# Kernel optimization log

Measured on AMD Instinct MI355X. Metric: run time of the kernel, lower is better.

## Reference

```python
import jax, jax.numpy as jnp
import numpy as np

VOCAB, D, PATCH, ROUNDS = 256, 64, 4, 3
B, T = 32, 8192


def setup_inputs() -> dict:
    key = jax.random.key(0)
    ks = jax.random.split(key, 16)
    s = 0.02
    inp = {
        "x": jax.random.randint(ks[0], (B, T), 0, VOCAB),
        "emb": jax.random.normal(ks[1], (VOCAB, D), jnp.float32) * s,
        # msg_net: Linear(2d->d), GELU, Linear(d->d); weights stored [in, out]
        "w_m1": jax.random.normal(ks[2], (2 * D, D), jnp.float32) * s,
        "b_m1": jnp.zeros((D,), jnp.float32),
        "w_m2": jax.random.normal(ks[3], (D, D), jnp.float32) * s,
        "b_m2": jnp.zeros((D,), jnp.float32),
        # update_net: Linear(2d->d), GELU, Linear(d->d)
        "w_u1": jax.random.normal(ks[4], (2 * D, D), jnp.float32) * s,
        "b_u1": jnp.zeros((D,), jnp.float32),
        "w_u2": jax.random.normal(ks[5], (D, D), jnp.float32) * s,
        "b_u2": jnp.zeros((D,), jnp.float32),
        # LayerNorm(d)
        "ln_g": jnp.ones((D,), jnp.float32),
        "ln_b": jnp.zeros((D,), jnp.float32),
        # readout: Linear(d -> vocab)
        "w_r": jax.random.normal(ks[6], (D, VOCAB), jnp.float32) * s,
        "b_r": jnp.zeros((VOCAB,), jnp.float32),
    }
    return inp


def _mlp(z, w1, b1, w2, b2):
    h = jax.nn.gelu(z @ w1 + b1, approximate=False)  # torch nn.GELU default = exact erf
    return h @ w2 + b2


def _layernorm(h, g, b, eps=1e-5):
    mu = jnp.mean(h, axis=-1, keepdims=True)
    var = jnp.mean((h - mu) ** 2, axis=-1, keepdims=True)
    return (h - mu) / jnp.sqrt(var + eps) * g + b


def reference(x, emb, w_m1, b_m1, w_m2, b_m2, w_u1, b_u1, w_u2, b_u2, ln_g, ln_b, w_r, b_r):
    Bx, Tx = x.shape
    P = PATCH
    N = (Tx + P - 1) // P
    xp = jnp.pad(x, ((0, 0), (0, N * P - Tx)))  # pad token id 0
    h = emb[xp].reshape(Bx, N, P, D).mean(axis=2)  # [B, N, d] patch-node features
    for _ in range(ROUNDS):
        left = jnp.pad(h[:, :-1], ((0, 0), (1, 0), (0, 0)))  # shift-right along N
        msgs = _mlp(jnp.concatenate([h, left], axis=-1), w_m1, b_m1, w_m2, b_m2)
        upd = _mlp(jnp.concatenate([h, msgs], axis=-1), w_u1, b_u1, w_u2, b_u2)
        h = _layernorm(h + upd, ln_g, ln_b)
    tok = jnp.repeat(h, P, axis=1)[:, :Tx]  # broadcast node feat to its P tokens
    return tok @ w_r + b_r  # [B, T, vocab]
```

## Files before the change

### kernel.cpp

```cpp
#include <hip/hip_runtime.h>
#include <hip/hip_bf16.h>
#include <math.h>

#define DD 64
#define NPB 2048
#define RTOT 65536
#define W1S 136
#define W2S 72

typedef __bf16 bf16;
typedef bf16 bf16x8 __attribute__((ext_vector_type(8)));
typedef float f32x4 __attribute__((ext_vector_type(4)));

#define COMPILER_FENCE() asm volatile("" ::: "memory")

__device__ __forceinline__ f32x4 mfma16(bf16x8 a, bf16x8 b, f32x4 c) {
  return __builtin_amdgcn_mfma_f32_16x16x32_bf16(a, b, c, 0, 0, 0);
}

__device__ __forceinline__ float gelu_exact(float x) {
  return 0.5f * x * (1.0f + erff(x * 0.70710678118654752f));
}

__device__ __forceinline__ bf16x8 cvt8(const float* p) {
  f32x4 a = *reinterpret_cast<const f32x4*>(p);
  f32x4 b = *reinterpret_cast<const f32x4*>(p + 4);
  bf16x8 r;
  r[0] = (bf16)a[0]; r[1] = (bf16)a[1]; r[2] = (bf16)a[2]; r[3] = (bf16)a[3];
  r[4] = (bf16)b[0]; r[5] = (bf16)b[1]; r[6] = (bf16)b[2]; r[7] = (bf16)b[3];
  return r;
}

__device__ __forceinline__ bf16x8 zero8() {
  bf16x8 z = {(bf16)0.f, (bf16)0.f, (bf16)0.f, (bf16)0.f,
              (bf16)0.f, (bf16)0.f, (bf16)0.f, (bf16)0.f};
  return z;
}

__global__ void __launch_bounds__(256) k_embed(const int* __restrict__ x,
                                               const float* __restrict__ emb,
                                               float* __restrict__ h) {
  int gid = blockIdx.x * 256 + threadIdx.x;
  int row = gid >> 6, d = gid & 63;
  const int* xp = x + row * 4;
  float s = 0.f;
#pragma unroll
  for (int p = 0; p < 4; ++p) s += emb[xp[p] * DD + d];
  h[row * DD + d] = s * 0.25f;
}

__global__ void __launch_bounds__(256) k_prep(const float* __restrict__ wm1,
                                              const float* __restrict__ wm2,
                                              const float* __restrict__ wu1,
                                              const float* __restrict__ wu2,
                                              bf16* __restrict__ Wsc) {
  int gid = blockIdx.x * 256 + threadIdx.x;
  if (gid < 8192) {
    int n = gid >> 7, k = gid & 127;
    Wsc[gid] = (bf16)wm1[k * 64 + n];
  } else if (gid < 16384) {
    int j = gid - 8192, n = j >> 7, k = j & 127;
    Wsc[gid] = (bf16)wu1[k * 64 + n];
  } else if (gid < 20480) {
    int j = gid - 16384, n = j >> 6, k = j & 63;
    Wsc[gid] = (bf16)wm2[k * 64 + n];
  } else {
    int j = gid - 20480, n = j >> 6, k = j & 63;
    Wsc[gid] = (bf16)wu2[k * 64 + n];
  }
}

__global__ void __launch_bounds__(256) k_prep_r(const float* __restrict__ wr,
                                                bf16* __restrict__ wrt) {
  int gid = blockIdx.x * 256 + threadIdx.x;
  int v = gid >> 6, k = gid & 63;
  wrt[gid] = (bf16)wr[k * 256 + v];
}

__global__ void __launch_bounds__(256) k_round_m(const float* __restrict__ hin,
                                                 float* __restrict__ hout,
                                                 const bf16* __restrict__ Wsc,
                                                 const float* __restrict__ bm1,
                                                 const float* __restrict__ bm2,
                                                 const float* __restrict__ bu1,
                                                 const float* __restrict__ bu2,
                                                 const float* __restrict__ lng,
                                                 const float* __restrict__ lnb) {
  __shared__ bf16 W1[2][64 * W1S];
  __shared__ bf16 Ms[64 * W2S];
  __shared__ bf16 Hs[64 * W2S];

  const int tid = threadIdx.x;
  const int lane = tid & 63;
  const int wv = tid >> 6;
  const int l15 = lane & 15;
  const int lhi = lane >> 4;
  const int rowbase = blockIdx.x * 64;

  for (int i = tid; i < 2048; i += 256) {
    int buf = i >> 10, idx = i & 1023;
    int n = idx >> 4, g = (idx & 15) * 8;
    *reinterpret_cast<bf16x8*>(&W1[buf][n * W1S + g]) =
        *reinterpret_cast<const bf16x8*>(Wsc + buf * 8192 + n * 128 + g);
  }
  bf16x8 fm2[4][2], fu2[4][2];
#pragma unroll
  for (int ct = 0; ct < 4; ++ct)
#pragma unroll
    for (int kt = 0; kt < 2; ++kt) {
      int off = (ct * 16 + l15) * 64 + kt * 32 + lhi * 8;
      fm2[ct][kt] = *reinterpret_cast<const bf16x8*>(Wsc + 16384 + off);
      fu2[ct][kt] = *reinterpret_cast<const bf16x8*>(Wsc + 20480 + off);
    }
  float bm1v[4], bm2v[4], bu1v[4], bu2v[4], lngv[4], lnbv[4];
#pragma unroll
  for (int ct = 0; ct < 4; ++ct) {
    int c = ct * 16 + l15;
    bm1v[ct] = bm1[c]; bm2v[ct] = bm2[c];
    bu1v[ct] = bu1[c]; bu2v[ct] = bu2[c];
    lngv[ct] = lng[c]; lnbv[ct] = lnb[c];
  }
  __syncthreads();

  const int lrow = wv * 16 + l15;
  const int grow = rowbase + lrow;
  const float* hrow = hin + (size_t)grow * DD;

  bf16x8 ah0 = cvt8(hrow + lhi * 8);
  bf16x8 ah1 = cvt8(hrow + 32 + lhi * 8);
  bf16x8 al0 = zero8(), al1 = zero8();
  if ((grow & (NPB - 1)) != 0) {
    al0 = cvt8(hrow - DD + lhi * 8);
    al1 = cvt8(hrow - DD + 32 + lhi * 8);
  }

  f32x4 acc[4];
  const f32x4 fz = {0.f, 0.f, 0.f, 0.f};

#pragma unroll
  for (int ct = 0; ct < 4; ++ct) acc[ct] = fz;
#pragma unroll
  for (int ct = 0; ct < 4; ++ct) {
    const bf16* wb = &W1[0][(ct * 16 + l15) * W1S];
    acc[ct] = mfma16(ah0, *reinterpret_cast<const bf16x8*>(wb + lhi * 8), acc[ct]);
    acc[ct] = mfma16(ah1, *reinterpret_cast<const bf16x8*>(wb + 32 + lhi * 8), acc[ct]);
    acc[ct] = mfma16(al0, *reinterpret_cast<const bf16x8*>(wb + 64 + lhi * 8), acc[ct]);
    acc[ct] = mfma16(al1, *reinterpret_cast<const bf16x8*>(wb + 96 + lhi * 8), acc[ct]);
  }
#pragma unroll
  for (int ct = 0; ct < 4; ++ct)
#pragma unroll
    for (int r = 0; r < 4; ++r) {
      float g = gelu_exact(acc[ct][r] + bm1v[ct]);
      Hs[(wv * 16 + lhi * 4 + r) * W2S + ct * 16 + l15] = (bf16)g;
    }
  COMPILER_FENCE();

#pragma unroll
  for (int ct = 0; ct < 4; ++ct) acc[ct] = fz;
  {
    bf16x8 g0 = *reinterpret_cast<const bf16x8*>(&Hs[lrow * W2S + lhi * 8]);
    bf16x8 g1 = *reinterpret_cast<const bf16x8*>(&Hs[lrow * W2S + 32 + lhi * 8]);
#pragma unroll
    for (int ct = 0; ct < 4; ++ct) {
      acc[ct] = mfma16(g0, fm2[ct][0], acc[ct]);
      acc[ct] = mfma16(g1, fm2[ct][1], acc[ct]);
    }
  }
#pragma unroll
  for (int ct = 0; ct < 4; ++ct)
#pragma unroll
    for (int r = 0; r < 4; ++r)
      Ms[(wv * 16 + lhi * 4 + r) * W2S + ct * 16 + l15] =
          (bf16)(acc[ct][r] + bm2v[ct]);
  COMPILER_FENCE();

#pragma unroll
  for (int ct = 0; ct < 4; ++ct) acc[ct] = fz;
  {
    bf16x8 m0 = *reinterpret_cast<const bf16x8*>(&Ms[lrow * W2S + lhi * 8]);
    bf16x8 m1 = *reinterpret_cast<const bf16x8*>(&Ms[lrow * W2S + 32 + lhi * 8]);
#pragma unroll
    for (int ct = 0; ct < 4; ++ct) {
      const bf16* wb = &W1[1][(ct * 16 + l15) * W1S];
      acc[ct] = mfma16(ah0, *reinterpret_cast<const bf16x8*>(wb + lhi * 8), acc[ct]);
      acc[ct] = mfma16(ah1, *reinterpret_cast<const bf16x8*>(wb + 32 + lhi * 8), acc[ct]);
      acc[ct] = mfma16(m0, *reinterpret_cast<const bf16x8*>(wb + 64 + lhi * 8), acc[ct]);
      acc[ct] = mfma16(m1, *reinterpret_cast<const bf16x8*>(wb + 96 + lhi * 8), acc[ct]);
    }
  }
  COMPILER_FENCE();
#pragma unroll
  for (int ct = 0; ct < 4; ++ct)
#pragma unroll
    for (int r = 0; r < 4; ++r) {
      float g = gelu_exact(acc[ct][r] + bu1v[ct]);
      Hs[(wv * 16 + lhi * 4 + r) * W2S + ct * 16 + l15] = (bf16)g;
    }
  COMPILER_FENCE();

#pragma unroll
  for (int ct = 0; ct < 4; ++ct) acc[ct] = fz;
  {
    bf16x8 u0 = *reinterpret_cast<const bf16x8*>(&Hs[lrow * W2S + lhi * 8]);
    bf16x8 u1 = *reinterpret_cast<const bf16x8*>(&Hs[lrow * W2S + 32 + lhi * 8]);
#pragma unroll
    for (int ct = 0; ct < 4; ++ct) {
      acc[ct] = mfma16(u0, fu2[ct][0], acc[ct]);
      acc[ct] = mfma16(u1, fu2[ct][1], acc[ct]);
    }
  }

  float xv[4][4];
#pragma unroll
  for (int ct = 0; ct < 4; ++ct)
#pragma unroll
    for (int r = 0; r < 4; ++r) {
      int row = rowbase + wv * 16 + lhi * 4 + r;
      xv[ct][r] = acc[ct][r] + bu2v[ct] + hin[row * DD + ct * 16 + l15];
    }
  float s1[4], s2[4];
#pragma unroll
  for (int r = 0; r < 4; ++r) {
    s1[r] = 0.f; s2[r] = 0.f;
#pragma unroll
    for (int ct = 0; ct < 4; ++ct) {
      s1[r] += xv[ct][r];
      s2[r] += xv[ct][r] * xv[ct][r];
    }
  }
#pragma unroll
  for (int off = 1; off < 16; off <<= 1)
#pragma unroll
    for (int r = 0; r < 4; ++r) {
      s1[r] += __shfl_xor(s1[r], off);
      s2[r] += __shfl_xor(s2[r], off);
    }
#pragma unroll
  for (int r = 0; r < 4; ++r) {
    float mu = s1[r] * 0.015625f;
    float var = s2[r] * 0.015625f - mu * mu;
    float rstd = rsqrtf(var + 1e-5f);
    int row = rowbase + wv * 16 + lhi * 4 + r;
#pragma unroll
    for (int ct = 0; ct < 4; ++ct)
      hout[row * DD + ct * 16 + l15] =
          (xv[ct][r] - mu) * rstd * lngv[ct] + lnbv[ct];
  }
}

__global__ void __launch_bounds__(256) k_readout(const float* __restrict__ h,
                                                 const bf16* __restrict__ wrt,
                                                 const float* __restrict__ br,
                                                 float* __restrict__ out) {
  __shared__ bf16 Wt[256 * W2S];
  const int tid = threadIdx.x, lane = tid & 63, wv = tid >> 6;
  const int l15 = lane & 15, lhi = lane >> 4;

  for (int i = tid; i < 2048; i += 256) {
    int v = i >> 3, g = (i & 7) * 8;
    *reinterpret_cast<bf16x8*>(&Wt[v * W2S + g]) =
        *reinterpret_cast<const bf16x8*>(wrt + v * 64 + g);
  }
  f32x4 brv[16];
#pragma unroll
  for (int vt = 0; vt < 16; ++vt)
    brv[vt] = *reinterpret_cast<const f32x4*>(br + vt * 16 + lhi * 4);
  __syncthreads();

  const int node = blockIdx.x * 64 + wv * 16 + l15;
  const float* hrow = h + (size_t)node * DD;
  bf16x8 b0 = cvt8(hrow + lhi * 8);
  bf16x8 b1 = cvt8(hrow + 32 + lhi * 8);

  f32x4 acc[16];
  const f32x4 fz = {0.f, 0.f, 0.f, 0.f};
#pragma unroll
  for (int vt = 0; vt < 16; ++vt) {
    const bf16* wb = &Wt[(vt * 16 + l15) * W2S];
    bf16x8 a0 = *reinterpret_cast<const bf16x8*>(wb + lhi * 8);
    bf16x8 a1 = *reinterpret_cast<const bf16x8*>(wb + 32 + lhi * 8);
    acc[vt] = mfma16(a0, b0, fz);
    acc[vt] = mfma16(a1, b1, acc[vt]);
  }

  float* ob = out + (size_t)node * 1024 + lhi * 4;
#pragma unroll
  for (int vt = 0; vt < 16; ++vt) {
    f32x4 val = acc[vt] + brv[vt];
    float* p = ob + vt * 16;
#pragma unroll
    for (int rep = 0; rep < 4; ++rep)
      *reinterpret_cast<f32x4*>(p + rep * 256) = val;
  }
}

extern "C" void kernel_launch(void* const* d_in, const int* in_sizes, int n_in,
                              void* d_out, int out_size, void* d_ws, size_t ws_size,
                              hipStream_t stream) {
  const int*   x   = (const int*)d_in[0];
  const float* emb = (const float*)d_in[1];
  const float* wm1 = (const float*)d_in[2];
  const float* bm1 = (const float*)d_in[3];
  const float* wm2 = (const float*)d_in[4];
  const float* bm2 = (const float*)d_in[5];
  const float* wu1 = (const float*)d_in[6];
  const float* bu1 = (const float*)d_in[7];
  const float* wu2 = (const float*)d_in[8];
  const float* bu2 = (const float*)d_in[9];
  const float* lng = (const float*)d_in[10];
  const float* lnb = (const float*)d_in[11];
  const float* wr  = (const float*)d_in[12];
  const float* br  = (const float*)d_in[13];
  float* out = (float*)d_out;

  char* ws = (char*)d_ws;
  float* ha = (float*)ws;
  float* hb = (float*)(ws + (size_t)RTOT * DD * 4);
  bf16* Wsc = (bf16*)d_out;
  bf16* wrt = (bf16*)ha;

  hipLaunchKernelGGL(k_prep, dim3(96), dim3(256), 0, stream,
                     wm1, wm2, wu1, wu2, Wsc);
  hipLaunchKernelGGL(k_embed, dim3(16384), dim3(256), 0, stream, x, emb, ha);
  hipLaunchKernelGGL(k_round_m, dim3(1024), dim3(256), 0, stream,
                     ha, hb, Wsc, bm1, bm2, bu1, bu2, lng, lnb);
  hipLaunchKernelGGL(k_round_m, dim3(1024), dim3(256), 0, stream,
                     hb, ha, Wsc, bm1, bm2, bu1, bu2, lng, lnb);
  hipLaunchKernelGGL(k_round_m, dim3(1024), dim3(256), 0, stream,
                     ha, hb, Wsc, bm1, bm2, bu1, bu2, lng, lnb);
  hipLaunchKernelGGL(k_prep_r, dim3(64), dim3(256), 0, stream, wr, wrt);
  hipLaunchKernelGGL(k_readout, dim3(1024), dim3(256), 0, stream, hb, wrt, br, out);
}
```

Before: 139.1 us.

## Fuse embed, three message-passing rounds and readout into one halo-tiled kernel

Replaces the separate embed, three round and readout kernels with a single kernel. Each block holds 80 node rows (64 outputs plus a 16-row left halo) in shared memory as bf16 across all rounds, so the per-round fp32 node features never go out to global memory and come back. In exchange, each block recomputes the halo rows, reloads the first-layer weights into shared memory twice per round behind extra barriers, and runs the readout on only 4 of 5 waves in two halves. Weight preparation, including the readout weights, is merged into one prep kernel that writes to workspace.

Result: slower. 156.1 us (+12.2%).

```diff
diff --git a/kernel.cpp b/kernel.cpp
--- a/kernel.cpp
+++ b/kernel.cpp
@@ -7,6 +7,8 @@
 #define RTOT 65536
 #define W1S 136
 #define W2S 72
+#define HBS 136
+#define TROWS 80
 
 typedef __bf16 bf16;
 typedef bf16 bf16x8 __attribute__((ext_vector_type(8)));
@@ -22,13 +24,8 @@
   return 0.5f * x * (1.0f + erff(x * 0.70710678118654752f));
 }
 
-__device__ __forceinline__ bf16x8 cvt8(const float* p) {
-  f32x4 a = *reinterpret_cast<const f32x4*>(p);
-  f32x4 b = *reinterpret_cast<const f32x4*>(p + 4);
-  bf16x8 r;
-  r[0] = (bf16)a[0]; r[1] = (bf16)a[1]; r[2] = (bf16)a[2]; r[3] = (bf16)a[3];
-  r[4] = (bf16)b[0]; r[5] = (bf16)b[1]; r[6] = (bf16)b[2]; r[7] = (bf16)b[3];
-  return r;
+__device__ __forceinline__ bf16x8 ld8(const bf16* p) {
+  return *reinterpret_cast<const bf16x8*>(p);
 }
 
 __device__ __forceinline__ bf16x8 zero8() {
@@ -37,22 +34,11 @@
   return z;
 }
 
-__global__ void __launch_bounds__(256) k_embed(const int* __restrict__ x,
-                                               const float* __restrict__ emb,
-                                               float* __restrict__ h) {
-  int gid = blockIdx.x * 256 + threadIdx.x;
-  int row = gid >> 6, d = gid & 63;
-  const int* xp = x + row * 4;
-  float s = 0.f;
-#pragma unroll
-  for (int p = 0; p < 4; ++p) s += emb[xp[p] * DD + d];
-  h[row * DD + d] = s * 0.25f;
-}
-
 __global__ void __launch_bounds__(256) k_prep(const float* __restrict__ wm1,
                                               const float* __restrict__ wm2,
                                               const float* __restrict__ wu1,
                                               const float* __restrict__ wu2,
+                                              const float* __restrict__ wr,
                                               bf16* __restrict__ Wsc) {
   int gid = blockIdx.x * 256 + threadIdx.x;
   if (gid < 8192) {
@@ -64,54 +50,47 @@
   } else if (gid < 20480) {
     int j = gid - 16384, n = j >> 6, k = j & 63;
     Wsc[gid] = (bf16)wm2[k * 64 + n];
-  } else {
+  } else if (gid < 24576) {
     int j = gid - 20480, n = j >> 6, k = j & 63;
     Wsc[gid] = (bf16)wu2[k * 64 + n];
-  }
-}
-
-__global__ void __launch_bounds__(256) k_prep_r(const float* __restrict__ wr,
-                                                bf16* __restrict__ wrt) {
-  int gid = blockIdx.x * 256 + threadIdx.x;
-  int v = gid >> 6, k = gid & 63;
-  wrt[gid] = (bf16)wr[k * 256 + v];
-}
-
-__global__ void __launch_bounds__(256) k_round_m(const float* __restrict__ hin,
-                                                 float* __restrict__ hout,
-                                                 const bf16* __restrict__ Wsc,
-                                                 const float* __restrict__ bm1,
-                                                 const float* __restrict__ bm2,
-                                                 const float* __restrict__ bu1,
-                                                 const float* __restrict__ bu2,
-                                                 const float* __restrict__ lng,
-                                                 const float* __restrict__ lnb) {
-  __shared__ bf16 W1[2][64 * W1S];
-  __shared__ bf16 Ms[64 * W2S];
-  __shared__ bf16 Hs[64 * W2S];
+  } else {
+    int j = gid - 24576, v = j >> 6, k = j & 63;
+    Wsc[gid] = (bf16)wr[k * 256 + v];
+  }
+}
+
+__global__ void __launch_bounds__(320) k_fused(const int* __restrict__ x,
+                                               const float* __restrict__ emb,
+                                               const bf16* __restrict__ Wsc,
+                                               const float* __restrict__ bm1,
+                                               const float* __restrict__ bm2,
+                                               const float* __restrict__ bu1,
+                                               const float* __restrict__ bu2,
+                                               const float* __restrict__ lng,
+                                               const float* __restrict__ lnb,
+                                               const float* __restrict__ br,
+                                               float* __restrict__ out) {
+  __shared__ __align__(16) char arena[50688];
+  bf16* Hs = (bf16*)arena;
+  bf16* W1 = (bf16*)(arena + 11520);
+  bf16* Hb = (bf16*)(arena + 28928);
+  bf16* Wt = (bf16*)arena;
+
+  const bf16* wm1t = Wsc;
+  const bf16* wu1t = Wsc + 8192;
+  const bf16* wm2t = Wsc + 16384;
+  const bf16* wu2t = Wsc + 20480;
+  const bf16* wrt  = Wsc + 24576;
 
   const int tid = threadIdx.x;
   const int lane = tid & 63;
   const int wv = tid >> 6;
   const int l15 = lane & 15;
   const int lhi = lane >> 4;
-  const int rowbase = blockIdx.x * 64;
-
-  for (int i = tid; i < 2048; i += 256) {
-    int buf = i >> 10, idx = i & 1023;
-    int n = idx >> 4, g = (idx & 15) * 8;
-    *reinterpret_cast<bf16x8*>(&W1[buf][n * W1S + g]) =
-        *reinterpret_cast<const bf16x8*>(Wsc + buf * 8192 + n * 128 + g);
-  }
-  bf16x8 fm2[4][2], fu2[4][2];
-#pragma unroll
-  for (int ct = 0; ct < 4; ++ct)
-#pragma unroll
-    for (int kt = 0; kt < 2; ++kt) {
-      int off = (ct * 16 + l15) * 64 + kt * 32 + lhi * 8;
-      fm2[ct][kt] = *reinterpret_cast<const bf16x8*>(Wsc + 16384 + off);
-      fu2[ct][kt] = *reinterpret_cast<const bf16x8*>(Wsc + 20480 + off);
-    }
+  const int rb = blockIdx.x * 64;
+  const int tr = wv * 16 + l15;
+  const int grow = rb - 16 + tr;
+
   float bm1v[4], bm2v[4], bu1v[4], bu2v[4], lngv[4], lnbv[4];
 #pragma unroll
   for (int ct = 0; ct < 4; ++ct) {
@@ -120,178 +99,195 @@
     bu1v[ct] = bu1[c]; bu2v[ct] = bu2[c];
     lngv[ct] = lng[c]; lnbv[ct] = lnb[c];
   }
+
+  for (int i = tid; i < 1024; i += 320) {
+    int n = i >> 4, g = (i & 15) * 8;
+    *reinterpret_cast<bf16x8*>(&W1[n * W1S + g]) = ld8(wm1t + n * 128 + g);
+  }
+
+  float hreg[4][4];
+#pragma unroll
+  for (int r = 0; r < 4; ++r) {
+    int trr = wv * 16 + lhi * 4 + r;
+    int g = rb - 16 + trr;
+    int gx = g < 0 ? 0 : g;
+    const int* xp = x + gx * 4;
+    int t0 = xp[0] * DD, t1 = xp[1] * DD, t2 = xp[2] * DD, t3 = xp[3] * DD;
+#pragma unroll
+    for (int ct = 0; ct < 4; ++ct) {
+      int c = ct * 16 + l15;
+      float s = emb[t0 + c] + emb[t1 + c] + emb[t2 + c] + emb[t3 + c];
+      hreg[ct][r] = s * 0.25f;
+      Hb[trr * HBS + c] = (bf16)hreg[ct][r];
+    }
+  }
   __syncthreads();
-
-  const int lrow = wv * 16 + l15;
-  const int grow = rowbase + lrow;
-  const float* hrow = hin + (size_t)grow * DD;
-
-  bf16x8 ah0 = cvt8(hrow + lhi * 8);
-  bf16x8 ah1 = cvt8(hrow + 32 + lhi * 8);
-  bf16x8 al0 = zero8(), al1 = zero8();
-  if ((grow & (NPB - 1)) != 0) {
-    al0 = cvt8(hrow - DD + lhi * 8);
-    al1 = cvt8(hrow - DD + 32 + lhi * 8);
-  }
 
   f32x4 acc[4];
   const f32x4 fz = {0.f, 0.f, 0.f, 0.f};
 
-#pragma unroll
-  for (int ct = 0; ct < 4; ++ct) acc[ct] = fz;
-#pragma unroll
-  for (int ct = 0; ct < 4; ++ct) {
-    const bf16* wb = &W1[0][(ct * 16 + l15) * W1S];
-    acc[ct] = mfma16(ah0, *reinterpret_cast<const bf16x8*>(wb + lhi * 8), acc[ct]);
-    acc[ct] = mfma16(ah1, *reinterpret_cast<const bf16x8*>(wb + 32 + lhi * 8), acc[ct]);
-    acc[ct] = mfma16(al0, *reinterpret_cast<const bf16x8*>(wb + 64 + lhi * 8), acc[ct]);
-    acc[ct] = mfma16(al1, *reinterpret_cast<const bf16x8*>(wb + 96 + lhi * 8), acc[ct]);
-  }
-#pragma unroll
-  for (int ct = 0; ct < 4; ++ct)
+  for (int rd = 0; rd < 3; ++rd) {
+    bf16x8 ah0 = ld8(&Hb[tr * HBS + lhi * 8]);
+    bf16x8 ah1 = ld8(&Hb[tr * HBS + 32 + lhi * 8]);
+    bf16x8 al0 = zero8(), al1 = zero8();
+    if (tr != 0 && (grow & (NPB - 1)) != 0) {
+      al0 = ld8(&Hb[(tr - 1) * HBS + lhi * 8]);
+      al1 = ld8(&Hb[(tr - 1) * HBS + 32 + lhi * 8]);
+    }
+#pragma unroll
+    for (int ct = 0; ct < 4; ++ct) acc[ct] = fz;
+#pragma unroll
+    for (int ct = 0; ct < 4; ++ct) {
+      const bf16* wb = &W1[(ct * 16 + l15) * W1S];
+      acc[ct] = mfma16(ah0, ld8(wb + lhi * 8), acc[ct]);
+      acc[ct] = mfma16(ah1, ld8(wb + 32 + lhi * 8), acc[ct]);
+      acc[ct] = mfma16(al0, ld8(wb + 64 + lhi * 8), acc[ct]);
+      acc[ct] = mfma16(al1, ld8(wb + 96 + lhi * 8), acc[ct]);
+    }
+#pragma unroll
+    for (int ct = 0; ct < 4; ++ct)
+#pragma unroll
+      for (int r = 0; r < 4; ++r) {
+        float g = gelu_exact(acc[ct][r] + bm1v[ct]);
+        Hs[(wv * 16 + lhi * 4 + r) * W2S + ct * 16 + l15] = (bf16)g;
+      }
+    COMPILER_FENCE();
+
+    {
+      bf16x8 g0 = ld8(&Hs[tr * W2S + lhi * 8]);
+      bf16x8 g1 = ld8(&Hs[tr * W2S + 32 + lhi * 8]);
+#pragma unroll
+      for (int ct = 0; ct < 4; ++ct) acc[ct] = fz;
+#pragma unroll
+      for (int ct = 0; ct < 4; ++ct) {
+        bf16x8 f0 = ld8(wm2t + (ct * 16 + l15) * 64 + lhi * 8);
+        bf16x8 f1 = ld8(wm2t + (ct * 16 + l15) * 64 + 32 + lhi * 8);
+        acc[ct] = mfma16(g0, f0, acc[ct]);
+        acc[ct] = mfma16(g1, f1, acc[ct]);
+      }
+#pragma unroll
+      for (int ct = 0; ct < 4; ++ct)
+#pragma unroll
+        for (int r = 0; r < 4; ++r)
+          Hb[(wv * 16 + lhi * 4 + r) * HBS + 64 + ct * 16 + l15] =
+              (bf16)(acc[ct][r] + bm2v[ct]);
+    }
+    __syncthreads();
+    for (int i = tid; i < 1024; i += 320) {
+      int n = i >> 4, g = (i & 15) * 8;
+      *reinterpret_cast<bf16x8*>(&W1[n * W1S + g]) = ld8(wu1t + n * 128 + g);
+    }
+    __syncthreads();
+
+    {
+      bf16x8 m0 = ld8(&Hb[tr * HBS + 64 + lhi * 8]);
+      bf16x8 m1 = ld8(&Hb[tr * HBS + 96 + lhi * 8]);
+#pragma unroll
+      for (int ct = 0; ct < 4; ++ct) acc[ct] = fz;
+#pragma unroll
+      for (int ct = 0; ct < 4; ++ct) {
+        const bf16* wb = &W1[(ct * 16 + l15) * W1S];
+        acc[ct] = mfma16(ah0, ld8(wb + lhi * 8), acc[ct]);
+        acc[ct] = mfma16(ah1, ld8(wb + 32 + lhi * 8), acc[ct]);
+        acc[ct] = mfma16(m0, ld8(wb + 64 + lhi * 8), acc[ct]);
+        acc[ct] = mfma16(m1, ld8(wb + 96 + lhi * 8), acc[ct]);
+      }
+    }
+#pragma unroll
+    for (int ct = 0; ct < 4; ++ct)
+#pragma unroll
+      for (int r = 0; r < 4; ++r) {
+        float g = gelu_exact(acc[ct][r] + bu1v[ct]);
+        Hs[(wv * 16 + lhi * 4 + r) * W2S + ct * 16 + l15] = (bf16)g;
+      }
+    COMPILER_FENCE();
+
+    {
+      bf16x8 u0 = ld8(&Hs[tr * W2S + lhi * 8]);
+      bf16x8 u1 = ld8(&Hs[tr * W2S + 32 + lhi * 8]);
+#pragma unroll
+      for (int ct = 0; ct < 4; ++ct) acc[ct] = fz;
+#pragma unroll
+      for (int ct = 0; ct < 4; ++ct) {
+        bf16x8 f0 = ld8(wu2t + (ct * 16 + l15) * 64 + lhi * 8);
+        bf16x8 f1 = ld8(wu2t + (ct * 16 + l15) * 64 + 32 + lhi * 8);
+        acc[ct] = mfma16(u0, f0, acc[ct]);
+        acc[ct] = mfma16(u1, f1, acc[ct]);
+      }
+    }
+    float xv[4][4];
+#pragma unroll
+    for (int ct = 0; ct < 4; ++ct)
+#pragma unroll
+      for (int r = 0; r < 4; ++r)
+        xv[ct][r] = acc[ct][r] + bu2v[ct] + hreg[ct][r];
+    float s1[4], s2[4];
 #pragma unroll
     for (int r = 0; r < 4; ++r) {
-      float g = gelu_exact(acc[ct][r] + bm1v[ct]);
-      Hs[(wv * 16 + lhi * 4 + r) * W2S + ct * 16 + l15] = (bf16)g;
-    }
-  COMPILER_FENCE();
-
-#pragma unroll
-  for (int ct = 0; ct < 4; ++ct) acc[ct] = fz;
-  {
-    bf16x8 g0 = *reinterpret_cast<const bf16x8*>(&Hs[lrow * W2S + lhi * 8]);
-    bf16x8 g1 = *reinterpret_cast<const bf16x8*>(&Hs[lrow * W2S + 32 + lhi * 8]);
-#pragma unroll
-    for (int ct = 0; ct < 4; ++ct) {
-      acc[ct] = mfma16(g0, fm2[ct][0], acc[ct]);
-      acc[ct] = mfma16(g1, fm2[ct][1], acc[ct]);
-    }
-  }
-#pragma unroll
-  for (int ct = 0; ct < 4; ++ct)
-#pragma unroll
-    for (int r = 0; r < 4; ++r)
-      Ms[(wv * 16 + lhi * 4 + r) * W2S + ct * 16 + l15] =
-          (bf16)(acc[ct][r] + bm2v[ct]);
-  COMPILER_FENCE();
-
-#pragma unroll
-  for (int ct = 0; ct < 4; ++ct) acc[ct] = fz;
-  {
-    bf16x8 m0 = *reinterpret_cast<const bf16x8*>(&Ms[lrow * W2S + lhi * 8]);
-    bf16x8 m1 = *reinterpret_cast<const bf16x8*>(&Ms[lrow * W2S + 32 + lhi * 8]);
-#pragma unroll
-    for (int ct = 0; ct < 4; ++ct) {
-      const bf16* wb = &W1[1][(ct * 16 + l15) * W1S];
-      acc[ct] = mfma16(ah0, *reinterpret_cast<const bf16x8*>(wb + lhi * 8), acc[ct]);
-      acc[ct] = mfma16(ah1, *reinterpret_cast<const bf16x8*>(wb + 32 + lhi * 8), acc[ct]);
-      acc[ct] = mfma16(m0, *reinterpret_cast<const bf16x8*>(wb + 64 + lhi * 8), acc[ct]);
-      acc[ct] = mfma16(m1, *reinterpret_cast<const bf16x8*>(wb + 96 + lhi * 8), acc[ct]);
-    }
-  }
-  COMPILER_FENCE();
-#pragma unroll
-  for (int ct = 0; ct < 4; ++ct)
+      s1[r] = 0.f; s2[r] = 0.f;
+#pragma unroll
+      for (int ct = 0; ct < 4; ++ct) {
+        s1[r] += xv[ct][r];
+        s2[r] += xv[ct][r] * xv[ct][r];
+      }
+    }
+#pragma unroll
+    for (int off = 1; off < 16; off <<= 1)
+#pragma unroll
+      for (int r = 0; r < 4; ++r) {
+        s1[r] += __shfl_xor(s1[r], off);
+        s2[r] += __shfl_xor(s2[r], off);
+      }
 #pragma unroll
     for (int r = 0; r < 4; ++r) {
-      float g = gelu_exact(acc[ct][r] + bu1v[ct]);
-      Hs[(wv * 16 + lhi * 4 + r) * W2S + ct * 16 + l15] = (bf16)g;
-    }
-  COMPILER_FENCE();
-
-#pragma unroll
-  for (int ct = 0; ct < 4; ++ct) acc[ct] = fz;
-  {
-    bf16x8 u0 = *reinterpret_cast<const bf16x8*>(&Hs[lrow * W2S + lhi * 8]);
-    bf16x8 u1 = *reinterpret_cast<const bf16x8*>(&Hs[lrow * W2S + 32 + lhi * 8]);
-#pragma unroll
-    for (int ct = 0; ct < 4; ++ct) {
-      acc[ct] = mfma16(u0, fu2[ct][0], acc[ct]);
-      acc[ct] = mfma16(u1, fu2[ct][1], acc[ct]);
-    }
-  }
-
-  float xv[4][4];
-#pragma unroll
-  for (int ct = 0; ct < 4; ++ct)
-#pragma unroll
-    for (int r = 0; r < 4; ++r) {
-      int row = rowbase + wv * 16 + lhi * 4 + r;
-      xv[ct][r] = acc[ct][r] + bu2v[ct] + hin[row * DD + ct * 16 + l15];
-    }
-  float s1[4], s2[4];
-#pragma unroll
-  for (int r = 0; r < 4; ++r) {
-    s1[r] = 0.f; s2[r] = 0.f;
-#pragma unroll
-    for (int ct = 0; ct < 4; ++ct) {
-      s1[r] += xv[ct][r];
-      s2[r] += xv[ct][r] * xv[ct][r];
-    }
-  }
-#pragma unroll
-  for (int off = 1; off < 16; off <<= 1)
-#pragma unroll
-    for (int r = 0; r < 4; ++r) {
-      s1[r] += __shfl_xor(s1[r], off);
-      s2[r] += __shfl_xor(s2[r], off);
-    }
-#pragma unroll
-  for (int r = 0; r < 4; ++r) {
-    float mu = s1[r] * 0.015625f;
-    float var = s2[r] * 0.015625f - mu * mu;
-    float rstd = rsqrtf(var + 1e-5f);
-    int row = rowbase + wv * 16 + lhi * 4 + r;
-#pragma unroll
-    for (int ct = 0; ct < 4; ++ct)
-      hout[row * DD + ct * 16 + l15] =
-          (xv[ct][r] - mu) * rstd * lngv[ct] + lnbv[ct];
-  }
-}
-
-__global__ void __launch_bounds__(256) k_readout(const float* __restrict__ h,
-                                                 const bf16* __restrict__ wrt,
-                                                 const float* __restrict__ br,
-                                                 float* __restrict__ out) {
-  __shared__ bf16 Wt[256 * W2S];
-  const int tid = threadIdx.x, lane = tid & 63, wv = tid >> 6;
-  const int l15 = lane & 15, lhi = lane >> 4;
-
-  for (int i = tid; i < 2048; i += 256) {
-    int v = i >> 3, g = (i & 7) * 8;
-    *reinterpret_cast<bf16x8*>(&Wt[v * W2S + g]) =
-        *reinterpret_cast<const bf16x8*>(wrt + v * 64 + g);
-  }
-  f32x4 brv[16];
-#pragma unroll
-  for (int vt = 0; vt < 16; ++vt)
-    brv[vt] = *reinterpret_cast<const f32x4*>(br + vt * 16 + lhi * 4);
-  __syncthreads();
-
-  const int node = blockIdx.x * 64 + wv * 16 + l15;
-  const float* hrow = h + (size_t)node * DD;
-  bf16x8 b0 = cvt8(hrow + lhi * 8);
-  bf16x8 b1 = cvt8(hrow + 32 + lhi * 8);
-
-  f32x4 acc[16];
-  const f32x4 fz = {0.f, 0.f, 0.f, 0.f};
-#pragma unroll
-  for (int vt = 0; vt < 16; ++vt) {
-    const bf16* wb = &Wt[(vt * 16 + l15) * W2S];
-    bf16x8 a0 = *reinterpret_cast<const bf16x8*>(wb + lhi * 8);
-    bf16x8 a1 = *reinterpret_cast<const bf16x8*>(wb + 32 + lhi * 8);
-    acc[vt] = mfma16(a0, b0, fz);
-    acc[vt] = mfma16(a1, b1, acc[vt]);
-  }
-
-  float* ob = out + (size_t)node * 1024 + lhi * 4;
-#pragma unroll
-  for (int vt = 0; vt < 16; ++vt) {
-    f32x4 val = acc[vt] + brv[vt];
-    float* p = ob + vt * 16;
-#pragma unroll
-    for (int rep = 0; rep < 4; ++rep)
-      *reinterpret_cast<f32x4*>(p + rep * 256) = val;
+      float mu = s1[r] * 0.015625f;
+      float var = s2[r] * 0.015625f - mu * mu;
+      float rstd = rsqrtf(var + 1e-5f);
+      int trr = wv * 16 + lhi * 4 + r;
+#pragma unroll
+      for (int ct = 0; ct < 4; ++ct) {
+        float o = (xv[ct][r] - mu) * rstd * lngv[ct] + lnbv[ct];
+        hreg[ct][r] = o;
+        Hb[trr * HBS + ct * 16 + l15] = (bf16)o;
+      }
+    }
+    __syncthreads();
+    if (rd < 2) {
+      for (int i = tid; i < 1024; i += 320) {
+        int n = i >> 4, g = (i & 15) * 8;
+        *reinterpret_cast<bf16x8*>(&W1[n * W1S + g]) = ld8(wm1t + n * 128 + g);
+      }
+      __syncthreads();
+    }
+  }
+
+  const int node = rb + (wv - 1) * 16 + l15;
+  bf16x8 b0 = ld8(&Hb[tr * HBS + lhi * 8]);
+  bf16x8 b1 = ld8(&Hb[tr * HBS + 32 + lhi * 8]);
+
+#pragma unroll
+  for (int half = 0; half < 2; ++half) {
+    for (int i = tid; i < 1024; i += 320) {
+      int v = i >> 3, g = (i & 7) * 8;
+      *reinterpret_cast<bf16x8*>(&Wt[v * W2S + g]) =
+          ld8(wrt + half * 8192 + v * 64 + g);
+    }
+    __syncthreads();
+    if (wv >= 1) {
+#pragma unroll
+      for (int vt = 0; vt < 8; ++vt) {
+        const bf16* wb = &Wt[(vt * 16 + l15) * W2S];
+        f32x4 a = mfma16(ld8(wb + lhi * 8), b0, fz);
+        a = mfma16(ld8(wb + 32 + lhi * 8), b1, a);
+        f32x4 brv = *reinterpret_cast<const f32x4*>(br + half * 128 + vt * 16 + lhi * 4);
+        f32x4 val = a + brv;
+        float* p = out + (size_t)node * 1024 + half * 128 + vt * 16 + lhi * 4;
+#pragma unroll
+        for (int rep = 0; rep < 4; ++rep)
+          *reinterpret_cast<f32x4*>(p + rep * 256) = val;
+      }
+    }
+    __syncthreads();
   }
 }
 
@@ -314,21 +310,10 @@
   const float* br  = (const float*)d_in[13];
   float* out = (float*)d_out;
 
-  char* ws = (char*)d_ws;
-  float* ha = (float*)ws;
-  float* hb = (float*)(ws + (size_t)RTOT * DD * 4);
-  bf16* Wsc = (bf16*)d_out;
-  bf16* wrt = (bf16*)ha;
-
-  hipLaunchKernelGGL(k_prep, dim3(96), dim3(256), 0, stream,
-                     wm1, wm2, wu1, wu2, Wsc);
-  hipLaunchKernelGGL(k_embed, dim3(16384), dim3(256), 0, stream, x, emb, ha);
-  hipLaunchKernelGGL(k_round_m, dim3(1024), dim3(256), 0, stream,
-                     ha, hb, Wsc, bm1, bm2, bu1, bu2, lng, lnb);
-  hipLaunchKernelGGL(k_round_m, dim3(1024), dim3(256), 0, stream,
-                     hb, ha, Wsc, bm1, bm2, bu1, bu2, lng, lnb);
-  hipLaunchKernelGGL(k_round_m, dim3(1024), dim3(256), 0, stream,
-                     ha, hb, Wsc, bm1, bm2, bu1, bu2, lng, lnb);
-  hipLaunchKernelGGL(k_prep_r, dim3(64), dim3(256), 0, stream, wr, wrt);
-  hipLaunchKernelGGL(k_readout, dim3(1024), dim3(256), 0, stream, hb, wrt, br, out);
-}
+  bf16* Wsc = (bf16*)d_ws;
+
+  hipLaunchKernelGGL(k_prep, dim3(160), dim3(256), 0, stream,
+                     wm1, wm2, wu1, wu2, wr, Wsc);
+  hipLaunchKernelGGL(k_fused, dim3(1024), dim3(320), 0, stream,
+                     x, emb, Wsc, bm1, bm2, bu1, bu2, lng, lnb, br, out);
+}
```
